# Performance work log

Hardware: AMD Instinct MI355X
Metric: run time of the kernel (lower is better)

Reference implementation:

```python
import jax, jax.numpy as jnp
import numpy as np

CLIP_MIN = 0.0  # recurrent_clip_min resolved in build() when -1
CLIP_MAX = 1.0  # recurrent_clip_max default when timesteps unknown


def setup_inputs() -> dict:
    key = jax.random.key(0)
    k1, k2, k3 = jax.random.split(key, 3)
    B, T, D, U = 64, 512, 256, 512
    x = jax.random.normal(k1, (B, T, D), dtype=jnp.float32)
    h0 = jnp.zeros((B, U), dtype=jnp.float32)
    W = jax.random.normal(k2, (D, U), dtype=jnp.float32) * (1.0 / np.sqrt(D))
    u = jax.random.uniform(k3, (U,), dtype=jnp.float32)  # uniform in clip range
    b = jnp.zeros((U,), dtype=jnp.float32)
    return {"x": x, "h0": h0, "W": W, "u": u, "b": b}


def reference(x, h0, W, u, b):
    # IndRNN: h_t = relu(x_t @ W + h_{t-1} * u + b), u clipped to [0, 1]
    u_c = jnp.clip(u, CLIP_MIN, CLIP_MAX)
    # One-time input projection for all timesteps: [B,T,U]
    proj = jnp.einsum("btd,du->btu", x, W) + b
    proj_t = jnp.swapaxes(proj, 0, 1)  # [T,B,U] for scan over time

    def step(h, p_t):
        h_new = jax.nn.relu(p_t + h * u_c)
        return h_new, h_new

    _, hs = jax.lax.scan(step, h0, proj_t)  # hs: [T,B,U]
    return jnp.swapaxes(hs, 0, 1)  # [B,T,U]
```

## Files before the change

### kernel.cpp

```cpp
#include <hip/hip_runtime.h>


typedef __bf16 bf16x8 __attribute__((ext_vector_type(8)));
typedef float f32x4 __attribute__((ext_vector_type(4)));

typedef const unsigned char __attribute__((address_space(1))) gc_t;
typedef unsigned char __attribute__((address_space(3))) lds_t;

__device__ __forceinline__ void gl_lds16(const void* g, void* l) {
    __builtin_amdgcn_global_load_lds((gc_t*)g, (lds_t*)l, 16, 0, 0);
}

__device__ __forceinline__ bf16x8 cvt8(f32x4 lo, f32x4 hi) {
    bf16x8 r;
    r[0] = (__bf16)lo[0]; r[1] = (__bf16)lo[1];
    r[2] = (__bf16)lo[2]; r[3] = (__bf16)lo[3];
    r[4] = (__bf16)hi[0]; r[5] = (__bf16)hi[1];
    r[6] = (__bf16)hi[2]; r[7] = (__bf16)hi[3];
    return r;
}

#define TC 64
#define GN 128

__global__ __launch_bounds__(256, 1) void indrnn_fused(
    const float* __restrict__ x,
    const float* __restrict__ W,
    const float* __restrict__ bias,
    const float* __restrict__ h0,
    const float* __restrict__ uvec,
    float* __restrict__ out,
    int B, int T, int U)
{
    __shared__ char Xs[2][TC * 1024];
    __shared__ char Ps[GN * TC * 4];

    const int tid  = threadIdx.x;
    const int lane = tid & 63;
    const int w    = tid >> 6;
    const int m    = lane & 15;
    const int quad = lane >> 4;
    const int b    = blockIdx.x;
    const int n0   = blockIdx.y * GN;
    const int tq   = (w >> 1) * 32;
    const int cq   = (w & 1) * 64;

    const float* xrow = x + (long)b * T * 256;

#pragma unroll
    for (int i = 0; i < 16; ++i) {
        int row = i * 4 + w;
        int sg  = lane ^ (row & 15);
        gl_lds16(xrow + (long)row * 256 + sg * 4, &Xs[0][row * 1024]);
    }

    bf16x8 bfr[4][8];
#pragma unroll
    for (int j = 0; j < 4; ++j)
#pragma unroll
        for (int kt = 0; kt < 8; ++kt) {
            const float* wp = W + (long)(kt * 32 + quad * 8) * U
                                + (n0 + cq + j * 16 + m);
            bf16x8 f;
#pragma unroll
            for (int e = 0; e < 8; ++e) f[e] = (__bf16)wp[(long)e * U];
            bfr[j][kt] = f;
        }

    float bb[4];
#pragma unroll
    for (int j = 0; j < 4; ++j) bb[j] = bias[n0 + cq + j * 16 + m];

    float uc = 0.0f, h = 0.0f;
    if (tid < GN) {
        uc = fminf(fmaxf(uvec[n0 + tid], 0.0f), 1.0f);
        h  = h0[(long)b * U + n0 + tid];
    }

    asm volatile("s_waitcnt vmcnt(0)" ::: "memory");
    __builtin_amdgcn_sched_barrier(0);
    __syncthreads();

    const int nch = T / TC;
    for (int c = 0; c < nch; ++c) {
        const int buf = c & 1;

        if (c + 1 < nch) {
            const float* gb = xrow + (long)(c + 1) * TC * 256;
#pragma unroll
            for (int i = 0; i < 16; ++i) {
                int row = i * 4 + w;
                int sg  = lane ^ (row & 15);
                gl_lds16(gb + (long)row * 256 + sg * 4, &Xs[buf ^ 1][row * 1024]);
            }
        }

        f32x4 acc[2][4];
#pragma unroll
        for (int i = 0; i < 2; ++i)
#pragma unroll
            for (int j = 0; j < 4; ++j) acc[i][j] = (f32x4){0.f, 0.f, 0.f, 0.f};

#pragma unroll
        for (int kt = 0; kt < 8; ++kt) {
            const int g0 = ((kt * 8 + quad * 2 + 0) ^ m) << 4;
            const int g1 = ((kt * 8 + quad * 2 + 1) ^ m) << 4;
            const char* r0p = Xs[buf] + (tq + m) * 1024;
            const char* r1p = Xs[buf] + (tq + 16 + m) * 1024;
            f32x4 a0lo = *(const f32x4*)(r0p + g0);
            f32x4 a0hi = *(const f32x4*)(r0p + g1);
            f32x4 a1lo = *(const f32x4*)(r1p + g0);
            f32x4 a1hi = *(const f32x4*)(r1p + g1);
            bf16x8 a0 = cvt8(a0lo, a0hi);
            bf16x8 a1 = cvt8(a1lo, a1hi);
#pragma unroll
            for (int j = 0; j < 4; ++j) {
                acc[0][j] = __builtin_amdgcn_mfma_f32_16x16x32_bf16(
                    a0, bfr[j][kt], acc[0][j], 0, 0, 0);
                acc[1][j] = __builtin_amdgcn_mfma_f32_16x16x32_bf16(
                    a1, bfr[j][kt], acc[1][j], 0, 0, 0);
            }
        }

#pragma unroll
        for (int i = 0; i < 2; ++i)
#pragma unroll
            for (int j = 0; j < 4; ++j) {
                f32x4 v = acc[i][j];
                f32x4 vb = {v[0] + bb[j], v[1] + bb[j], v[2] + bb[j], v[3] + bb[j]};
                int col = cq + j * 16 + m;
                int g   = (tq >> 2) + i * 4 + quad;
                *(f32x4*)(Ps + col * 256 + (((g ^ (col & 7)) << 4))) = vb;
            }
        __syncthreads();

        if (tid < GN) {
            f32x4 pv[16];
            const int ub = tid * 256;
            const int ux = (tid & 7) << 4;
#pragma unroll
            for (int gg = 0; gg < 16; ++gg)
                pv[gg] = *(const f32x4*)(Ps + ub + ((gg << 4) ^ ux));
            float* og = out + ((long)b * T + c * TC) * U + n0 + tid;
#pragma unroll
            for (int gg = 0; gg < 16; ++gg)
#pragma unroll
                for (int e = 0; e < 4; ++e) {
                    h = fmaxf(fmaf(h, uc, pv[gg][e]), 0.0f);
                    og[(long)(gg * 4 + e) * U] = h;
                }
        }

        if (tid < GN) {
            asm volatile("s_waitcnt vmcnt(48)" ::: "memory");
        } else {
            asm volatile("s_waitcnt vmcnt(0)" ::: "memory");
        }
        __builtin_amdgcn_sched_barrier(0);
        __syncthreads();
    }
}

#define BM 128
#define BN 128
#define BK 8

__global__ __launch_bounds__(256) void indrnn_gemm_bias(
    const float* __restrict__ A, const float* __restrict__ Bm,
    const float* __restrict__ bias, float* __restrict__ C,
    int M, int N, int K)
{
    __shared__ float As[BK][BM];
    __shared__ float Bs[BK][BN];
    const int tid = threadIdx.x;
    const int row0 = blockIdx.x * BM, col0 = blockIdx.y * BN;
    const int tx = tid & 15, ty = tid >> 4;
    float acc[8][8];
#pragma unroll
    for (int i = 0; i < 8; ++i)
#pragma unroll
        for (int j = 0; j < 8; ++j) acc[i][j] = 0.0f;
    const int am = tid >> 1, ak = (tid & 1) * 4;
    const int bk = tid >> 5, bn = (tid & 31) * 4;
    const float* Aptr = A + (long)(row0 + am) * K + ak;
    const float* Bptr = Bm + (long)bk * N + col0 + bn;
    for (int kt = 0; kt < K; kt += BK) {
        float4 av = *(const float4*)(Aptr + kt);
        float4 bv = *(const float4*)(Bptr + (long)kt * N);
        As[ak + 0][am] = av.x; As[ak + 1][am] = av.y;
        As[ak + 2][am] = av.z; As[ak + 3][am] = av.w;
        *(float4*)&Bs[bk][bn] = bv;
        __syncthreads();
#pragma unroll
        for (int k = 0; k < BK; ++k) {
            float4 a0 = *(const float4*)&As[k][ty * 4];
            float4 a1 = *(const float4*)&As[k][64 + ty * 4];
            float4 b0 = *(const float4*)&Bs[k][tx * 4];
            float4 b1 = *(const float4*)&Bs[k][64 + tx * 4];
            float a[8] = {a0.x, a0.y, a0.z, a0.w, a1.x, a1.y, a1.z, a1.w};
            float bb2[8] = {b0.x, b0.y, b0.z, b0.w, b1.x, b1.y, b1.z, b1.w};
#pragma unroll
            for (int i = 0; i < 8; ++i)
#pragma unroll
                for (int j = 0; j < 8; ++j)
                    acc[i][j] = fmaf(a[i], bb2[j], acc[i][j]);
        }
        __syncthreads();
    }
    float bb[8];
#pragma unroll
    for (int j = 0; j < 4; ++j) {
        bb[j] = bias[col0 + tx * 4 + j];
        bb[j + 4] = bias[col0 + 64 + tx * 4 + j];
    }
#pragma unroll
    for (int i = 0; i < 8; ++i) {
        const int r = (i < 4) ? (ty * 4 + i) : (64 + ty * 4 + (i - 4));
        float* crow = C + (long)(row0 + r) * N + col0;
        float4 v0 = {acc[i][0] + bb[0], acc[i][1] + bb[1], acc[i][2] + bb[2], acc[i][3] + bb[3]};
        float4 v1 = {acc[i][4] + bb[4], acc[i][5] + bb[5], acc[i][6] + bb[6], acc[i][7] + bb[7]};
        *(float4*)(crow + tx * 4) = v0;
        *(float4*)(crow + 64 + tx * 4) = v1;
    }
}

#define SCAN_UNROLL 32

__global__ __launch_bounds__(256) void indrnn_scan(
    float* __restrict__ out, const float* __restrict__ h0,
    const float* __restrict__ u, int B, int T, int U)
{
    const int idx = blockIdx.x * blockDim.x + threadIdx.x;
    if (idx >= B * U) return;
    const int b = idx / U;
    const int un = idx - b * U;
    const float uc = fminf(fmaxf(u[un], 0.0f), 1.0f);
    float h = h0[(long)b * U + un];
    float* p = out + (long)b * T * U + un;
    for (int t = 0; t < T; t += SCAN_UNROLL) {
        float pv[SCAN_UNROLL];
#pragma unroll
        for (int i = 0; i < SCAN_UNROLL; ++i)
            pv[i] = p[(long)(t + i) * U];
#pragma unroll
        for (int i = 0; i < SCAN_UNROLL; ++i) {
            h = fmaxf(fmaf(h, uc, pv[i]), 0.0f);
            pv[i] = h;
        }
#pragma unroll
        for (int i = 0; i < SCAN_UNROLL; ++i)
            p[(long)(t + i) * U] = pv[i];
    }
}

extern "C" void kernel_launch(void* const* d_in, const int* in_sizes, int n_in,
                              void* d_out, int out_size, void* d_ws, size_t ws_size,
                              hipStream_t stream) {
    const float* x  = (const float*)d_in[0];
    const float* h0 = (const float*)d_in[1];
    const float* W  = (const float*)d_in[2];
    const float* u  = (const float*)d_in[3];
    const float* b  = (const float*)d_in[4];
    float* out = (float*)d_out;

    const int U = in_sizes[3];
    const int B = in_sizes[1] / U;
    const int D = in_sizes[2] / U;
    const int T = in_sizes[0] / (B * D);
    const int M = B * T;

    const bool fused_ok = (D == 256) && (U % GN == 0) && (T % TC == 0);

    if (fused_ok) {
        dim3 g(B, U / GN);
        indrnn_fused<<<g, 256, 0, stream>>>(x, W, b, h0, u, out, B, T, U);
    } else {
        dim3 ggrid(M / BM, U / BN);
        indrnn_gemm_bias<<<ggrid, 256, 0, stream>>>(x, W, b, out, M, U, D);
        const int nthreads = B * U;
        indrnn_scan<<<(nthreads + 255) / 256, 256, 0, stream>>>(out, h0, u, B, T, U);
    }
}
```

Before: 121.8 us.

## Double block to 512 threads, splitting GEMM rows across eight waves

Each block of the fused IndRNN kernel now runs 8 waves instead of 4. Each wave computes one 16-row by 64-column tile instead of two 16-row tiles. The aim is to halve per-wave MFMA and LDS work per chunk and spread the global-to-LDS x loads over more waves, which shortens the projection phase before the serial scan. The cost is that each extra wave also holds a full register copy of the W fragments. The scan phase still uses only 128 threads, so the serial part is not shortened.

After: 136.5 us. 12.1% more time.

```diff
diff --git a/kernel.cpp b/kernel.cpp
--- a/kernel.cpp
+++ b/kernel.cpp
@@ -23,7 +23,7 @@
 #define TC 64
 #define GN 128
 
-__global__ __launch_bounds__(256, 1) void indrnn_fused(
+__global__ __launch_bounds__(512, 1) void indrnn_fused(
     const float* __restrict__ x,
     const float* __restrict__ W,
     const float* __restrict__ bias,
@@ -42,14 +42,14 @@
     const int quad = lane >> 4;
     const int b    = blockIdx.x;
     const int n0   = blockIdx.y * GN;
-    const int tq   = (w >> 1) * 32;
+    const int rq   = (w >> 1) * 16;
     const int cq   = (w & 1) * 64;
 
     const float* xrow = x + (long)b * T * 256;
 
 #pragma unroll
-    for (int i = 0; i < 16; ++i) {
-        int row = i * 4 + w;
+    for (int i = 0; i < 8; ++i) {
+        int row = i * 8 + w;
         int sg  = lane ^ (row & 15);
         gl_lds16(xrow + (long)row * 256 + sg * 4, &Xs[0][row * 1024]);
     }
@@ -88,50 +88,39 @@
         if (c + 1 < nch) {
             const float* gb = xrow + (long)(c + 1) * TC * 256;
 #pragma unroll
-            for (int i = 0; i < 16; ++i) {
-                int row = i * 4 + w;
+            for (int i = 0; i < 8; ++i) {
+                int row = i * 8 + w;
                 int sg  = lane ^ (row & 15);
                 gl_lds16(gb + (long)row * 256 + sg * 4, &Xs[buf ^ 1][row * 1024]);
             }
         }
 
-        f32x4 acc[2][4];
-#pragma unroll
-        for (int i = 0; i < 2; ++i)
-#pragma unroll
-            for (int j = 0; j < 4; ++j) acc[i][j] = (f32x4){0.f, 0.f, 0.f, 0.f};
+        f32x4 acc[4];
+#pragma unroll
+        for (int j = 0; j < 4; ++j) acc[j] = (f32x4){0.f, 0.f, 0.f, 0.f};
 
 #pragma unroll
         for (int kt = 0; kt < 8; ++kt) {
             const int g0 = ((kt * 8 + quad * 2 + 0) ^ m) << 4;
             const int g1 = ((kt * 8 + quad * 2 + 1) ^ m) << 4;
-            const char* r0p = Xs[buf] + (tq + m) * 1024;
-            const char* r1p = Xs[buf] + (tq + 16 + m) * 1024;
-            f32x4 a0lo = *(const f32x4*)(r0p + g0);
-            f32x4 a0hi = *(const f32x4*)(r0p + g1);
-            f32x4 a1lo = *(const f32x4*)(r1p + g0);
-            f32x4 a1hi = *(const f32x4*)(r1p + g1);
-            bf16x8 a0 = cvt8(a0lo, a0hi);
-            bf16x8 a1 = cvt8(a1lo, a1hi);
-#pragma unroll
-            for (int j = 0; j < 4; ++j) {
-                acc[0][j] = __builtin_amdgcn_mfma_f32_16x16x32_bf16(
-                    a0, bfr[j][kt], acc[0][j], 0, 0, 0);
-                acc[1][j] = __builtin_amdgcn_mfma_f32_16x16x32_bf16(
-                    a1, bfr[j][kt], acc[1][j], 0, 0, 0);
-            }
-        }
-
-#pragma unroll
-        for (int i = 0; i < 2; ++i)
-#pragma unroll
-            for (int j = 0; j < 4; ++j) {
-                f32x4 v = acc[i][j];
-                f32x4 vb = {v[0] + bb[j], v[1] + bb[j], v[2] + bb[j], v[3] + bb[j]};
-                int col = cq + j * 16 + m;
-                int g   = (tq >> 2) + i * 4 + quad;
-                *(f32x4*)(Ps + col * 256 + (((g ^ (col & 7)) << 4))) = vb;
-            }
+            const char* rp = Xs[buf] + (rq + m) * 1024;
+            f32x4 alo = *(const f32x4*)(rp + g0);
+            f32x4 ahi = *(const f32x4*)(rp + g1);
+            bf16x8 a = cvt8(alo, ahi);
+#pragma unroll
+            for (int j = 0; j < 4; ++j)
+                acc[j] = __builtin_amdgcn_mfma_f32_16x16x32_bf16(
+                    a, bfr[j][kt], acc[j], 0, 0, 0);
+        }
+
+#pragma unroll
+        for (int j = 0; j < 4; ++j) {
+            f32x4 v = acc[j];
+            f32x4 vb = {v[0] + bb[j], v[1] + bb[j], v[2] + bb[j], v[3] + bb[j]};
+            int col = cq + j * 16 + m;
+            int g   = (rq >> 2) + quad;
+            *(f32x4*)(Ps + col * 256 + (((g ^ (col & 7)) << 4))) = vb;
+        }
         __syncthreads();
 
         if (tid < GN) {
@@ -273,7 +262,7 @@
 
     if (fused_ok) {
         dim3 g(B, U / GN);
-        indrnn_fused<<<g, 256, 0, stream>>>(x, W, b, h0, u, out, B, T, U);
+        indrnn_fused<<<g, 512, 0, stream>>>(x, W, b, h0, u, out, B, T, U);
     } else {
         dim3 ggrid(M / BM, U / BN);
         indrnn_gemm_bias<<<ggrid, 256, 0, stream>>>(x, W, b, out, M, U, D);
```
